# Performance work log

Measured on AMD Instinct MI355X. Metric: run time of the kernel, lower is better.

The kernel has to match this reference:

```python
import jax, jax.numpy as jnp
import numpy as np

C = 51  # num_relation


def setup_inputs() -> dict:
    key = jax.random.key(0)
    N_o, N_u, D = 16384, 16384, 1024
    k = jax.random.split(key, 6)
    feat = jax.random.normal(k[0], (N_o + N_u, D), jnp.float32)
    # first N_o rows are labeled (label != 0), remaining N_u rows unlabeled (label == 0)
    label = jnp.concatenate([
        jax.random.randint(k[1], (N_o,), 1, C),
        jnp.zeros((N_u,), jnp.int32),
    ]).astype(jnp.int32)
    W_o = jax.random.normal(k[2], (C, D), jnp.float32) * 0.03
    b_o = jnp.zeros((C,), jnp.float32)
    W = jax.random.normal(k[3], (C, D), jnp.float32) * 0.03
    b = jnp.zeros((C,), jnp.float32)
    cls = jnp.arange(C)
    group_mid_mask = (cls >= 16) & (cls < 36)   # groups[1]
    group_tail_mask = cls >= 36                 # groups[2]
    # runtime torch.randint partner sampling, hoisted to input construction
    idx_m = jax.random.randint(k[4], (2, N_u), 0, N_o)  # 2 mid copies
    idx_t = jax.random.randint(k[5], (3, N_u), 0, N_o)  # 3 tail copies
    return dict(feat=feat, label=label, W_o=W_o, b_o=b_o, W=W, b=b,
                group_mid_mask=group_mid_mask, group_tail_mask=group_tail_mask,
                idx_m=idx_m, idx_t=idx_t)


def reference(feat, label, W_o, b_o, W, b, group_mid_mask, group_tail_mask, idx_m, idx_t):
    n_u = idx_m.shape[1]
    n_o = feat.shape[0] - n_u
    feat_o, feat_u = feat[:n_o], feat[n_o:]
    label_o = label[:n_o]

    # fc_o under no_grad, then softmax / top-1 rank + score
    logits = jax.lax.stop_gradient(feat_u @ W_o.T + b_o)      # [N_u, C]
    p = jax.nn.softmax(logits, axis=1)
    pred = jnp.argmax(p, axis=1)                               # ranks[:,0]
    score = jnp.max(p, axis=1)                                 # score[:,0]

    # group membership + confidence thresholds (heads are unused in the original)
    mid_m = group_mid_mask[pred] & (score > 0.5)
    tail_m = group_tail_mask[pred] & (score > 0.3)

    oh_u = jax.nn.one_hot(pred, C, dtype=feat.dtype)
    oh_o = jax.nn.one_hot(label_o, C, dtype=feat.dtype)

    im = idx_m.reshape(-1)   # [2*N_u]
    it = idx_t.reshape(-1)   # [3*N_u]

    fm = 0.7 * feat_o[im] + 0.3 * jnp.tile(feat_u, (2, 1))
    lm = 0.7 * oh_o[im] + 0.3 * jnp.tile(oh_u, (2, 1))
    ft = 0.7 * feat_o[it] + 0.3 * jnp.tile(feat_u, (3, 1))
    lt = 0.7 * oh_o[it] + 0.3 * jnp.tile(oh_u, (3, 1))

    feat_cat = jnp.concatenate([fm, ft], axis=0)               # [5*N_u, D]
    label_cat = jnp.concatenate([lm, lt], axis=0)              # [5*N_u, C]
    w = jnp.concatenate([jnp.tile(mid_m, 2), jnp.tile(tail_m, 3)]).astype(feat.dtype)

    # soft-label cross entropy on fc(feat_cat); masked mean over selected rows
    logp = jax.nn.log_softmax(feat_cat @ W.T + b, axis=1)
    ce = -(logp * label_cat).sum(axis=1)
    cnt = w.sum()
    return (ce * w).sum() / jnp.maximum(cnt, 1.0)
```

## Files before the change

### kernel.cpp

```cpp
#include <hip/hip_runtime.h>
#include <math.h>

#define DD 1024
#define SN 52
#define NU 16384
#define NO 16384
#define CEBLK 5120

typedef short short8 __attribute__((ext_vector_type(8)));
typedef float f32x4 __attribute__((ext_vector_type(4)));

__device__ __forceinline__ unsigned short f2b(float x) {
    unsigned int u = __float_as_uint(x);
    u += 0x7FFFu + ((u >> 16) & 1u);
    return (unsigned short)(u >> 16);
}

__device__ __forceinline__ short8 cvt8(float4 a, float4 b) {
    short8 r;
    r[0] = (short)f2b(a.x); r[1] = (short)f2b(a.y);
    r[2] = (short)f2b(a.z); r[3] = (short)f2b(a.w);
    r[4] = (short)f2b(b.x); r[5] = (short)f2b(b.y);
    r[6] = (short)f2b(b.z); r[7] = (short)f2b(b.w);
    return r;
}

__device__ __forceinline__ void gl_lds(const void* g, void* l) {
    __builtin_amdgcn_global_load_lds(
        (const __attribute__((address_space(1))) void*)g,
        (__attribute__((address_space(3))) void*)l, 16, 0, 0);
}

__global__ __launch_bounds__(256) void convW(const float* __restrict__ W,
                                             const float* __restrict__ W_o,
                                             unsigned short* __restrict__ Wcat) {
    const int n = blockIdx.x;
    const int k = threadIdx.x * 4;
    const float* src = nullptr;
    if (n < 64) { if (n < 51) src = W + (size_t)n * DD; }
    else        { if (n - 64 < 51) src = W_o + (size_t)(n - 64) * DD; }
    float4 v = src ? *(const float4*)(src + k) : make_float4(0.f, 0.f, 0.f, 0.f);
    ushort4 o;
    o.x = f2b(v.x); o.y = f2b(v.y); o.z = f2b(v.z); o.w = f2b(v.w);
    *(ushort4*)(Wcat + (size_t)n * DD + k) = o;
}

template <int IS_U>
__device__ __forceinline__ void gemm_body(const float* __restrict__ feat,
                                          const unsigned short* __restrict__ Wcat,
                                          const float* __restrict__ b_o,
                                          int m0, float* __restrict__ Bmat,
                                          int* __restrict__ flags, char* lds) {
    const int tid = threadIdx.x;
    const int lane = tid & 63;
    const int w = tid >> 6;
    const int m = lane & 15;
    const int quad = lane >> 4;
    const int s = m & 7;
    const int s2 = m & 3;

    const char *gs0, *gs1, *gs2;
    int lo0, lo1, lo2, st1;
    if constexpr (!IS_U) {
        { const int r = w * 16 + (lane >> 3);
          const int g = (lane & 7) ^ (r & 7);
          gs0 = (const char*)(feat + (size_t)(m0 + r) * DD + g * 4); lo0 = (w * 2) * 1024; }
        { const int r = w * 16 + 8 + (lane >> 3);
          const int g = (lane & 7) ^ (r & 7);
          gs1 = (const char*)(feat + (size_t)(m0 + r) * DD + g * 4); lo1 = (w * 2 + 1) * 1024; }
        { const int r = w * 16 + (lane >> 2);
          const int g = (lane & 3) ^ (r & 3);
          gs2 = (const char*)(Wcat + (size_t)r * DD + g * 8); lo2 = 8192 + w * 1024; }
        st1 = 128;
    } else {
        { const int r = w * 8 + (lane >> 3);
          const int g = (lane & 7) ^ (r & 7);
          gs0 = (const char*)(feat + (size_t)(NO + m0 + r) * DD + g * 4); lo0 = w * 1024; }
        { const int r = (w * 2) * 16 + (lane >> 2);
          const int g = (lane & 3) ^ (r & 3);
          gs1 = (const char*)(Wcat + (size_t)r * DD + g * 8); lo1 = 4096 + (w * 2) * 1024; }
        { const int r = (w * 2 + 1) * 16 + (lane >> 2);
          const int g = (lane & 3) ^ (r & 3);
          gs2 = (const char*)(Wcat + (size_t)r * DD + g * 8); lo2 = 4096 + (w * 2 + 1) * 1024; }
        st1 = 64;
    }

    f32x4 acc[4];
#pragma unroll
    for (int nf = 0; nf < 4; ++nf) acc[nf] = (f32x4){0.f, 0.f, 0.f, 0.f};

    const int rA = (IS_U ? (w & 1) * 16 : w * 16) + m;
    const int rBbase = (IS_U ? (w >> 1) * 64 : 0) + m;
    const int Bofs = IS_U ? 4096 : 8192;

#define STAGE(t, buf)                                  \
    do {                                               \
        gl_lds(gs0 + (size_t)(t) * 128, (buf) + lo0);  \
        gl_lds(gs1 + (size_t)(t) * st1, (buf) + lo1);  \
        gl_lds(gs2 + (size_t)(t) * 64,  (buf) + lo2);  \
    } while (0)

    STAGE(0, lds);
    STAGE(1, lds + 12288);

    int bc = 0;
    for (int kt = 0; kt < 32; ++kt) {
        if (kt < 30) {
            const int bi2 = (bc == 0) ? 2 : bc - 1;
            STAGE(kt + 2, lds + bi2 * 12288);
            asm volatile("s_waitcnt vmcnt(6)\n\ts_barrier" ::: "memory");
        } else if (kt == 30) {
            asm volatile("s_waitcnt vmcnt(3)\n\ts_barrier" ::: "memory");
        } else {
            asm volatile("s_waitcnt vmcnt(0)\n\ts_barrier" ::: "memory");
        }
        const char* buf = lds + bc * 12288;
        const float4 f0 = *(const float4*)(buf + rA * 128 + ((2 * quad) ^ s) * 16);
        const float4 f1 = *(const float4*)(buf + rA * 128 + ((2 * quad + 1) ^ s) * 16);
        const short8 af = cvt8(f0, f1);
#pragma unroll
        for (int nf = 0; nf < 4; ++nf) {
            const short8 bf =
                *(const short8*)(buf + Bofs + (rBbase + nf * 16) * 64 + (quad ^ s2) * 16);
            acc[nf] = __builtin_amdgcn_mfma_f32_16x16x32_bf16(af, bf, acc[nf], 0, 0, 0);
        }
        bc = (bc == 2) ? 0 : bc + 1;
    }
#undef STAGE

    if constexpr (!IS_U) {
        const int rbase = m0 + w * 16 + quad * 4;
#pragma unroll
        for (int nf = 0; nf < 4; ++nf) {
            const int col = nf * 16 + m;
            if (col < 51) {
#pragma unroll
                for (int r = 0; r < 4; ++r)
                    Bmat[(size_t)(rbase + r) * SN + col] = acc[nf][r];
            }
        }
    } else {
        const int wm = w & 1, wn = w >> 1;
        const int rloc = m0 + wm * 16 + quad * 4;
        if (wn == 0) {
#pragma unroll
            for (int nf = 0; nf < 4; ++nf) {
                const int col = nf * 16 + m;
                if (col < 51) {
#pragma unroll
                    for (int r = 0; r < 4; ++r)
                        Bmat[(size_t)(NO + rloc + r) * SN + col] = acc[nf][r];
                }
            }
        } else {
            float boc[4];
#pragma unroll
            for (int c = 0; c < 4; ++c) {
                const int col = c * 16 + m;
                boc[c] = (col < 51) ? b_o[col] : 0.f;
            }
#pragma unroll
            for (int r = 0; r < 4; ++r) {
                float z[4];
                float mx = acc[0][r] + boc[0];
                int mi = m;
                z[0] = mx;
#pragma unroll
                for (int c = 1; c < 4; ++c) {
                    const int col = c * 16 + m;
                    z[c] = (col < 51) ? acc[c][r] + boc[c] : -INFINITY;
                    if (z[c] > mx) { mx = z[c]; mi = col; }
                }
#pragma unroll
                for (int off = 1; off < 16; off <<= 1) {
                    const float om = __shfl_xor(mx, off);
                    const int oi = __shfl_xor(mi, off);
                    if (om > mx || (om == mx && oi < mi)) { mx = om; mi = oi; }
                }
                float e = 0.f;
#pragma unroll
                for (int c = 0; c < 4; ++c)
                    if (c * 16 + m < 51) e += expf(z[c] - mx);
#pragma unroll
                for (int off = 1; off < 16; off <<= 1) e += __shfl_xor(e, off);
                const float score = 1.f / e;
                const int mid = (mi >= 16 && mi < 36 && score > 0.5f) ? 1 : 0;
                const int tail = (mi >= 36 && score > 0.3f) ? 1 : 0;
                if (m == 0) flags[rloc + r] = mi | (mid << 8) | (tail << 9);
            }
        }
    }
}

__global__ __launch_bounds__(256, 4) void gemm_mfma(const float* __restrict__ feat,
                                                    const unsigned short* __restrict__ Wcat,
                                                    const float* __restrict__ b_o,
                                                    float* __restrict__ Bmat,
                                                    int* __restrict__ flags) {
    __shared__ __attribute__((aligned(16))) char lds[3 * 12288];
    if (blockIdx.x < 256)
        gemm_body<0>(feat, Wcat, b_o, blockIdx.x * 64, Bmat, flags, lds);
    else
        gemm_body<1>(feat, Wcat, b_o, (blockIdx.x - 256) * 32, Bmat, flags, lds);
}

__global__ __launch_bounds__(256) void cekernel(const float* __restrict__ B,
                                                const float* __restrict__ bb,
                                                const int* __restrict__ label,
                                                const int* __restrict__ idxm,
                                                const int* __restrict__ idxt,
                                                const int* __restrict__ flags,
                                                double* __restrict__ pnum,
                                                int* __restrict__ pcnt) {
    __shared__ float snum[4];
    __shared__ int scnt[4];
    const int w = threadIdx.x >> 6;
    const int lane = threadIdx.x & 63;
    float csum = 0.f;
    int ccnt = 0;
#pragma unroll
    for (int it = 0; it < 4; ++it) {
        const int j = (blockIdx.x * 4 + w) * 4 + it;
        int u, o, active;
        if (j < 2 * NU) {
            u = j & (NU - 1);
            o = idxm[j];
            active = (flags[u] >> 8) & 1;
        } else {
            const int j2 = j - 2 * NU;
            u = j2 & (NU - 1);
            o = idxt[j2];
            active = (flags[u] >> 9) & 1;
        }
        if (active) {
            const float* Bo = B + (size_t)o * SN;
            const float* Bu = B + (size_t)(NO + u) * SN;
            float z = -INFINITY;
            if (lane < 51) z = 0.7f * Bo[lane] + 0.3f * Bu[lane] + bb[lane];
            float m = z;
#pragma unroll
            for (int off = 1; off < 64; off <<= 1) m = fmaxf(m, __shfl_xor(m, off));
            float e = (lane < 51) ? expf(z - m) : 0.f;
#pragma unroll
            for (int off = 1; off < 64; off <<= 1) e += __shfl_xor(e, off);
            const float lse = m + logf(e);
            const int lo = label[o];
            const int pu = flags[u] & 255;
            const float zlo = __shfl(z, lo);
            const float zpu = __shfl(z, pu);
            csum += lse - 0.7f * zlo - 0.3f * zpu;
            ccnt += 1;
        }
    }
    if (lane == 0) { snum[w] = csum; scnt[w] = ccnt; }
    __syncthreads();
    if (threadIdx.x == 0) {
        pnum[blockIdx.x] = (double)snum[0] + (double)snum[1] +
                           (double)snum[2] + (double)snum[3];
        pcnt[blockIdx.x] = scnt[0] + scnt[1] + scnt[2] + scnt[3];
    }
}

__global__ __launch_bounds__(256) void finalize(const double* __restrict__ pnum,
                                                const int* __restrict__ pcnt,
                                                float* __restrict__ out) {
    __shared__ double sd[4];
    __shared__ int sc[4];
    const int w = threadIdx.x >> 6;
    const int lane = threadIdx.x & 63;
    double s = 0.0;
    int c = 0;
    for (int i = threadIdx.x; i < CEBLK; i += 256) {
        s += pnum[i];
        c += pcnt[i];
    }
#pragma unroll
    for (int off = 1; off < 64; off <<= 1) {
        s += __shfl_xor(s, off);
        c += __shfl_xor(c, off);
    }
    if (lane == 0) { sd[w] = s; sc[w] = c; }
    __syncthreads();
    if (threadIdx.x == 0) {
        const double n = sd[0] + sd[1] + sd[2] + sd[3];
        const int cc = sc[0] + sc[1] + sc[2] + sc[3];
        out[0] = (float)(n / (cc > 1 ? (double)cc : 1.0));
    }
}

extern "C" void kernel_launch(void* const* d_in, const int* in_sizes, int n_in,
                              void* d_out, int out_size, void* d_ws, size_t ws_size,
                              hipStream_t stream) {
    const float* feat = (const float*)d_in[0];
    const int* label = (const int*)d_in[1];
    const float* W_o = (const float*)d_in[2];
    const float* b_o = (const float*)d_in[3];
    const float* W = (const float*)d_in[4];
    const float* b = (const float*)d_in[5];
    const int* idxm = (const int*)d_in[8];
    const int* idxt = (const int*)d_in[9];

    char* ws = (char*)d_ws;
    float* Bmat = (float*)ws;
    double* pnum = (double*)(ws + 6815744);
    int* pcnt = (int*)(ws + 6815744 + 40960);
    int* flags = (int*)(ws + 6815744 + 40960 + 20480);
    unsigned short* Wcat =
        (unsigned short*)(ws + 6815744 + 40960 + 20480 + 65536);

    convW<<<128, 256, 0, stream>>>(W, W_o, Wcat);
    gemm_mfma<<<768, 256, 0, stream>>>(feat, Wcat, b_o, Bmat, flags);
    cekernel<<<CEBLK, 256, 0, stream>>>(Bmat, b, label, idxm, idxt, flags, pnum, pcnt);
    finalize<<<1, 256, 0, stream>>>(pnum, pcnt, (float*)d_out);
}
```

Before: 237.2 us.

## Project only labeled rows referenced by active mixup pairs; ballot-compact CE work

Splits the fused GEMM into an unlabeled-row pass and a labeled-row pass. The unlabeled pass computes pseudo-labels and flags, then uses an atomic bitmap to build a deduplicated list of labeled rows that active mid/tail pairs actually reference. The labeled GEMM then gathers and projects only those rows instead of all 16384. The CE kernel now assigns one pair per lane and walks only the active lanes via a ballot mask, which cuts its block count. This adds atomics, an extra launch, and a gather with data-dependent work in exchange for skipping projections of unreferenced rows.

After: 243.7 us. +2.8%, slower.

```diff
diff --git a/kernel.cpp b/kernel.cpp
--- a/kernel.cpp
+++ b/kernel.cpp
@@ -5,7 +5,7 @@
 #define SN 52
 #define NU 16384
 #define NO 16384
-#define CEBLK 5120
+#define NCEB 320
 
 typedef short short8 __attribute__((ext_vector_type(8)));
 typedef float f32x4 __attribute__((ext_vector_type(4)));
@@ -33,7 +33,14 @@
 
 __global__ __launch_bounds__(256) void convW(const float* __restrict__ W,
                                              const float* __restrict__ W_o,
-                                             unsigned short* __restrict__ Wcat) {
+                                             unsigned short* __restrict__ Wcat,
+                                             unsigned int* __restrict__ bitmap,
+                                             int* __restrict__ cnt) {
+    if (blockIdx.x == 0) {
+        bitmap[threadIdx.x] = 0u;
+        bitmap[threadIdx.x + 256] = 0u;
+        if (threadIdx.x == 0) cnt[0] = 0;
+    }
     const int n = blockIdx.x;
     const int k = threadIdx.x * 4;
     const float* src = nullptr;
@@ -45,12 +52,18 @@
     *(ushort4*)(Wcat + (size_t)n * DD + k) = o;
 }
 
-template <int IS_U>
-__device__ __forceinline__ void gemm_body(const float* __restrict__ feat,
-                                          const unsigned short* __restrict__ Wcat,
-                                          const float* __restrict__ b_o,
-                                          int m0, float* __restrict__ Bmat,
-                                          int* __restrict__ flags, char* lds) {
+__global__ __launch_bounds__(256, 4) void gemm_u(const float* __restrict__ feat,
+                                                 const unsigned short* __restrict__ Wcat,
+                                                 const float* __restrict__ b_o,
+                                                 float* __restrict__ Bmat,
+                                                 int* __restrict__ flags,
+                                                 const int* __restrict__ idxm,
+                                                 const int* __restrict__ idxt,
+                                                 unsigned int* __restrict__ bitmap,
+                                                 int* __restrict__ cnt,
+                                                 int* __restrict__ listo) {
+    __shared__ __attribute__((aligned(16))) char lds[3 * 12288];
+    const int m0 = blockIdx.x * 32;
     const int tid = threadIdx.x;
     const int lane = tid & 63;
     const int w = tid >> 6;
@@ -60,54 +73,39 @@
     const int s2 = m & 3;
 
     const char *gs0, *gs1, *gs2;
-    int lo0, lo1, lo2, st1;
-    if constexpr (!IS_U) {
-        { const int r = w * 16 + (lane >> 3);
-          const int g = (lane & 7) ^ (r & 7);
-          gs0 = (const char*)(feat + (size_t)(m0 + r) * DD + g * 4); lo0 = (w * 2) * 1024; }
-        { const int r = w * 16 + 8 + (lane >> 3);
-          const int g = (lane & 7) ^ (r & 7);
-          gs1 = (const char*)(feat + (size_t)(m0 + r) * DD + g * 4); lo1 = (w * 2 + 1) * 1024; }
-        { const int r = w * 16 + (lane >> 2);
-          const int g = (lane & 3) ^ (r & 3);
-          gs2 = (const char*)(Wcat + (size_t)r * DD + g * 8); lo2 = 8192 + w * 1024; }
-        st1 = 128;
-    } else {
-        { const int r = w * 8 + (lane >> 3);
-          const int g = (lane & 7) ^ (r & 7);
-          gs0 = (const char*)(feat + (size_t)(NO + m0 + r) * DD + g * 4); lo0 = w * 1024; }
-        { const int r = (w * 2) * 16 + (lane >> 2);
-          const int g = (lane & 3) ^ (r & 3);
-          gs1 = (const char*)(Wcat + (size_t)r * DD + g * 8); lo1 = 4096 + (w * 2) * 1024; }
-        { const int r = (w * 2 + 1) * 16 + (lane >> 2);
-          const int g = (lane & 3) ^ (r & 3);
-          gs2 = (const char*)(Wcat + (size_t)r * DD + g * 8); lo2 = 4096 + (w * 2 + 1) * 1024; }
-        st1 = 64;
-    }
+    int lo0, lo1, lo2;
+    { const int r = w * 8 + (lane >> 3);
+      const int g = (lane & 7) ^ (r & 7);
+      gs0 = (const char*)(feat + (size_t)(NO + m0 + r) * DD + g * 4); lo0 = w * 1024; }
+    { const int r = (w * 2) * 16 + (lane >> 2);
+      const int g = (lane & 3) ^ (r & 3);
+      gs1 = (const char*)(Wcat + (size_t)r * DD + g * 8); lo1 = 4096 + (w * 2) * 1024; }
+    { const int r = (w * 2 + 1) * 16 + (lane >> 2);
+      const int g = (lane & 3) ^ (r & 3);
+      gs2 = (const char*)(Wcat + (size_t)r * DD + g * 8); lo2 = 4096 + (w * 2 + 1) * 1024; }
 
     f32x4 acc[4];
 #pragma unroll
     for (int nf = 0; nf < 4; ++nf) acc[nf] = (f32x4){0.f, 0.f, 0.f, 0.f};
 
-    const int rA = (IS_U ? (w & 1) * 16 : w * 16) + m;
-    const int rBbase = (IS_U ? (w >> 1) * 64 : 0) + m;
-    const int Bofs = IS_U ? 4096 : 8192;
-
-#define STAGE(t, buf)                                  \
+    const int rA = (w & 1) * 16 + m;
+    const int rBbase = (w >> 1) * 64 + m;
+
+#define STAGEU(t, buf)                                 \
     do {                                               \
         gl_lds(gs0 + (size_t)(t) * 128, (buf) + lo0);  \
-        gl_lds(gs1 + (size_t)(t) * st1, (buf) + lo1);  \
+        gl_lds(gs1 + (size_t)(t) * 64,  (buf) + lo1);  \
         gl_lds(gs2 + (size_t)(t) * 64,  (buf) + lo2);  \
     } while (0)
 
-    STAGE(0, lds);
-    STAGE(1, lds + 12288);
+    STAGEU(0, lds);
+    STAGEU(1, lds + 12288);
 
     int bc = 0;
     for (int kt = 0; kt < 32; ++kt) {
         if (kt < 30) {
             const int bi2 = (bc == 0) ? 2 : bc - 1;
-            STAGE(kt + 2, lds + bi2 * 12288);
+            STAGEU(kt + 2, lds + bi2 * 12288);
             asm volatile("s_waitcnt vmcnt(6)\n\ts_barrier" ::: "memory");
         } else if (kt == 30) {
             asm volatile("s_waitcnt vmcnt(3)\n\ts_barrier" ::: "memory");
@@ -121,87 +119,167 @@
 #pragma unroll
         for (int nf = 0; nf < 4; ++nf) {
             const short8 bf =
-                *(const short8*)(buf + Bofs + (rBbase + nf * 16) * 64 + (quad ^ s2) * 16);
+                *(const short8*)(buf + 4096 + (rBbase + nf * 16) * 64 + (quad ^ s2) * 16);
             acc[nf] = __builtin_amdgcn_mfma_f32_16x16x32_bf16(af, bf, acc[nf], 0, 0, 0);
         }
         bc = (bc == 2) ? 0 : bc + 1;
     }
-#undef STAGE
-
-    if constexpr (!IS_U) {
-        const int rbase = m0 + w * 16 + quad * 4;
+#undef STAGEU
+
+    const int wm = w & 1, wn = w >> 1;
+    const int rloc = m0 + wm * 16 + quad * 4;
+    if (wn == 0) {
 #pragma unroll
         for (int nf = 0; nf < 4; ++nf) {
             const int col = nf * 16 + m;
             if (col < 51) {
 #pragma unroll
                 for (int r = 0; r < 4; ++r)
-                    Bmat[(size_t)(rbase + r) * SN + col] = acc[nf][r];
+                    Bmat[(size_t)(NO + rloc + r) * SN + col] = acc[nf][r];
             }
         }
     } else {
-        const int wm = w & 1, wn = w >> 1;
-        const int rloc = m0 + wm * 16 + quad * 4;
-        if (wn == 0) {
-#pragma unroll
-            for (int nf = 0; nf < 4; ++nf) {
-                const int col = nf * 16 + m;
-                if (col < 51) {
-#pragma unroll
-                    for (int r = 0; r < 4; ++r)
-                        Bmat[(size_t)(NO + rloc + r) * SN + col] = acc[nf][r];
+        float boc[4];
+#pragma unroll
+        for (int c = 0; c < 4; ++c) {
+            const int col = c * 16 + m;
+            boc[c] = (col < 51) ? b_o[col] : 0.f;
+        }
+#pragma unroll
+        for (int r = 0; r < 4; ++r) {
+            float z[4];
+            float mx = acc[0][r] + boc[0];
+            int mi = m;
+            z[0] = mx;
+#pragma unroll
+            for (int c = 1; c < 4; ++c) {
+                const int col = c * 16 + m;
+                z[c] = (col < 51) ? acc[c][r] + boc[c] : -INFINITY;
+                if (z[c] > mx) { mx = z[c]; mi = col; }
+            }
+#pragma unroll
+            for (int off = 1; off < 16; off <<= 1) {
+                const float om = __shfl_xor(mx, off);
+                const int oi = __shfl_xor(mi, off);
+                if (om > mx || (om == mx && oi < mi)) { mx = om; mi = oi; }
+            }
+            float e = 0.f;
+#pragma unroll
+            for (int c = 0; c < 4; ++c)
+                if (c * 16 + m < 51) e += expf(z[c] - mx);
+#pragma unroll
+            for (int off = 1; off < 16; off <<= 1) e += __shfl_xor(e, off);
+            const float score = 1.f / e;
+            const int mid = (mi >= 16 && mi < 36 && score > 0.5f) ? 1 : 0;
+            const int tail = (mi >= 36 && score > 0.3f) ? 1 : 0;
+            if (m == 0) flags[rloc + r] = mi | (mid << 8) | (tail << 9);
+            const int nref = mid ? 2 : (tail ? 3 : 0);
+            if (m < nref) {
+                const int u = rloc + r;
+                const int oo = mid ? idxm[(size_t)m * NU + u]
+                                   : idxt[(size_t)m * NU + u];
+                const unsigned bit = 1u << (oo & 31);
+                const unsigned old = atomicOr(&bitmap[oo >> 5], bit);
+                if (!(old & bit)) {
+                    const int p = atomicAdd(cnt, 1);
+                    listo[p] = oo;
                 }
             }
+        }
+    }
+}
+
+__global__ __launch_bounds__(256, 4) void gemm_o(const float* __restrict__ feat,
+                                                 const unsigned short* __restrict__ Wcat,
+                                                 float* __restrict__ Bmat,
+                                                 const int* __restrict__ cnt,
+                                                 const int* __restrict__ listo) {
+    const int n = cnt[0];
+    const int base = blockIdx.x * 64;
+    if (base >= n) return;
+    __shared__ __attribute__((aligned(16))) char lds[3 * 12288];
+    const int nm1 = n - 1;
+    const int tid = threadIdx.x;
+    const int lane = tid & 63;
+    const int w = tid >> 6;
+    const int m = lane & 15;
+    const int quad = lane >> 4;
+    const int s = m & 7;
+    const int s2 = m & 3;
+
+    const char *gs0, *gs1, *gs2;
+    int lo0, lo1, lo2;
+    { const int r = w * 16 + (lane >> 3);
+      const int g = (lane & 7) ^ (r & 7);
+      int li = base + r; if (li > nm1) li = nm1;
+      const int gr = listo[li];
+      gs0 = (const char*)(feat + (size_t)gr * DD + g * 4); lo0 = (w * 2) * 1024; }
+    { const int r = w * 16 + 8 + (lane >> 3);
+      const int g = (lane & 7) ^ (r & 7);
+      int li = base + r; if (li > nm1) li = nm1;
+      const int gr = listo[li];
+      gs1 = (const char*)(feat + (size_t)gr * DD + g * 4); lo1 = (w * 2 + 1) * 1024; }
+    { const int r = w * 16 + (lane >> 2);
+      const int g = (lane & 3) ^ (r & 3);
+      gs2 = (const char*)(Wcat + (size_t)r * DD + g * 8); lo2 = 8192 + w * 1024; }
+
+    f32x4 acc[4];
+#pragma unroll
+    for (int nf = 0; nf < 4; ++nf) acc[nf] = (f32x4){0.f, 0.f, 0.f, 0.f};
+
+    const int rA = w * 16 + m;
+
+#define STAGEO(t, buf)                                 \
+    do {                                               \
+        gl_lds(gs0 + (size_t)(t) * 128, (buf) + lo0);  \
+        gl_lds(gs1 + (size_t)(t) * 128, (buf) + lo1);  \
+        gl_lds(gs2 + (size_t)(t) * 64,  (buf) + lo2);  \
+    } while (0)
+
+    STAGEO(0, lds);
+    STAGEO(1, lds + 12288);
+
+    int bc = 0;
+    for (int kt = 0; kt < 32; ++kt) {
+        if (kt < 30) {
+            const int bi2 = (bc == 0) ? 2 : bc - 1;
+            STAGEO(kt + 2, lds + bi2 * 12288);
+            asm volatile("s_waitcnt vmcnt(6)\n\ts_barrier" ::: "memory");
+        } else if (kt == 30) {
+            asm volatile("s_waitcnt vmcnt(3)\n\ts_barrier" ::: "memory");
         } else {
-            float boc[4];
-#pragma unroll
-            for (int c = 0; c < 4; ++c) {
-                const int col = c * 16 + m;
-                boc[c] = (col < 51) ? b_o[col] : 0.f;
-            }
-#pragma unroll
-            for (int r = 0; r < 4; ++r) {
-                float z[4];
-                float mx = acc[0][r] + boc[0];
-                int mi = m;
-                z[0] = mx;
-#pragma unroll
-                for (int c = 1; c < 4; ++c) {
-                    const int col = c * 16 + m;
-                    z[c] = (col < 51) ? acc[c][r] + boc[c] : -INFINITY;
-                    if (z[c] > mx) { mx = z[c]; mi = col; }
-                }
-#pragma unroll
-                for (int off = 1; off < 16; off <<= 1) {
-                    const float om = __shfl_xor(mx, off);
-                    const int oi = __shfl_xor(mi, off);
-                    if (om > mx || (om == mx && oi < mi)) { mx = om; mi = oi; }
-                }
-                float e = 0.f;
-#pragma unroll
-                for (int c = 0; c < 4; ++c)
-                    if (c * 16 + m < 51) e += expf(z[c] - mx);
-#pragma unroll
-                for (int off = 1; off < 16; off <<= 1) e += __shfl_xor(e, off);
-                const float score = 1.f / e;
-                const int mid = (mi >= 16 && mi < 36 && score > 0.5f) ? 1 : 0;
-                const int tail = (mi >= 36 && score > 0.3f) ? 1 : 0;
-                if (m == 0) flags[rloc + r] = mi | (mid << 8) | (tail << 9);
-            }
-        }
-    }
-}
-
-__global__ __launch_bounds__(256, 4) void gemm_mfma(const float* __restrict__ feat,
-                                                    const unsigned short* __restrict__ Wcat,
-                                                    const float* __restrict__ b_o,
-                                                    float* __restrict__ Bmat,
-                                                    int* __restrict__ flags) {
-    __shared__ __attribute__((aligned(16))) char lds[3 * 12288];
-    if (blockIdx.x < 256)
-        gemm_body<0>(feat, Wcat, b_o, blockIdx.x * 64, Bmat, flags, lds);
-    else
-        gemm_body<1>(feat, Wcat, b_o, (blockIdx.x - 256) * 32, Bmat, flags, lds);
+            asm volatile("s_waitcnt vmcnt(0)\n\ts_barrier" ::: "memory");
+        }
+        const char* buf = lds + bc * 12288;
+        const float4 f0 = *(const float4*)(buf + rA * 128 + ((2 * quad) ^ s) * 16);
+        const float4 f1 = *(const float4*)(buf + rA * 128 + ((2 * quad + 1) ^ s) * 16);
+        const short8 af = cvt8(f0, f1);
+#pragma unroll
+        for (int nf = 0; nf < 4; ++nf) {
+            const short8 bf =
+                *(const short8*)(buf + 8192 + (m + nf * 16) * 64 + (quad ^ s2) * 16);
+            acc[nf] = __builtin_amdgcn_mfma_f32_16x16x32_bf16(af, bf, acc[nf], 0, 0, 0);
+        }
+        bc = (bc == 2) ? 0 : bc + 1;
+    }
+#undef STAGEO
+
+    const int rl = w * 16 + quad * 4;
+    int grow[4];
+#pragma unroll
+    for (int r = 0; r < 4; ++r) {
+        int li = base + rl + r; if (li > nm1) li = nm1;
+        grow[r] = listo[li];
+    }
+#pragma unroll
+    for (int nf = 0; nf < 4; ++nf) {
+        const int col = nf * 16 + m;
+        if (col < 51) {
+#pragma unroll
+            for (int r = 0; r < 4; ++r)
+                Bmat[(size_t)grow[r] * SN + col] = acc[nf][r];
+        }
+    }
 }
 
 __global__ __launch_bounds__(256) void cekernel(const float* __restrict__ B,
@@ -216,43 +294,48 @@
     __shared__ int scnt[4];
     const int w = threadIdx.x >> 6;
     const int lane = threadIdx.x & 63;
-    float csum = 0.f;
+    const int j = (blockIdx.x * 4 + w) * 64 + lane;
+    int u, o, fl, act;
+    if (j < 2 * NU) {
+        u = j & (NU - 1);
+        fl = flags[u];
+        act = (fl >> 8) & 1;
+        o = idxm[j];
+    } else {
+        const int j2 = j - 2 * NU;
+        u = j2 & (NU - 1);
+        fl = flags[u];
+        act = (fl >> 9) & 1;
+        o = idxt[j2];
+    }
+    const float bbv = (lane < 51) ? bb[lane] : 0.f;
+    unsigned long long mask = __ballot(act);
+    float fsum = 0.f;
     int ccnt = 0;
-#pragma unroll
-    for (int it = 0; it < 4; ++it) {
-        const int j = (blockIdx.x * 4 + w) * 4 + it;
-        int u, o, active;
-        if (j < 2 * NU) {
-            u = j & (NU - 1);
-            o = idxm[j];
-            active = (flags[u] >> 8) & 1;
-        } else {
-            const int j2 = j - 2 * NU;
-            u = j2 & (NU - 1);
-            o = idxt[j2];
-            active = (flags[u] >> 9) & 1;
-        }
-        if (active) {
-            const float* Bo = B + (size_t)o * SN;
-            const float* Bu = B + (size_t)(NO + u) * SN;
-            float z = -INFINITY;
-            if (lane < 51) z = 0.7f * Bo[lane] + 0.3f * Bu[lane] + bb[lane];
-            float m = z;
-#pragma unroll
-            for (int off = 1; off < 64; off <<= 1) m = fmaxf(m, __shfl_xor(m, off));
-            float e = (lane < 51) ? expf(z - m) : 0.f;
-#pragma unroll
-            for (int off = 1; off < 64; off <<= 1) e += __shfl_xor(e, off);
-            const float lse = m + logf(e);
-            const int lo = label[o];
-            const int pu = flags[u] & 255;
-            const float zlo = __shfl(z, lo);
-            const float zpu = __shfl(z, pu);
-            csum += lse - 0.7f * zlo - 0.3f * zpu;
-            ccnt += 1;
-        }
-    }
-    if (lane == 0) { snum[w] = csum; scnt[w] = ccnt; }
+    while (mask) {
+        const int b = (int)__builtin_ctzll(mask);
+        mask &= mask - 1;
+        const int ob = __shfl(o, b);
+        const int ub = __shfl(u, b);
+        const int pu = __shfl(fl, b) & 255;
+        float z = -INFINITY;
+        if (lane < 51)
+            z = 0.7f * B[(size_t)ob * SN + lane] +
+                0.3f * B[(size_t)(NO + ub) * SN + lane] + bbv;
+        float mx = z;
+#pragma unroll
+        for (int off = 1; off < 64; off <<= 1) mx = fmaxf(mx, __shfl_xor(mx, off));
+        float e = (lane < 51) ? expf(z - mx) : 0.f;
+#pragma unroll
+        for (int off = 1; off < 64; off <<= 1) e += __shfl_xor(e, off);
+        const float lse = mx + logf(e);
+        const int lo = label[ob];
+        const float zlo = __shfl(z, lo);
+        const float zpu = __shfl(z, pu);
+        fsum += lse - 0.7f * zlo - 0.3f * zpu;
+        ++ccnt;
+    }
+    if (lane == 0) { snum[w] = fsum; scnt[w] = ccnt; }
     __syncthreads();
     if (threadIdx.x == 0) {
         pnum[blockIdx.x] = (double)snum[0] + (double)snum[1] +
@@ -270,7 +353,7 @@
     const int lane = threadIdx.x & 63;
     double s = 0.0;
     int c = 0;
-    for (int i = threadIdx.x; i < CEBLK; i += 256) {
+    for (int i = threadIdx.x; i < NCEB; i += 256) {
         s += pnum[i];
         c += pcnt[i];
     }
@@ -303,13 +386,17 @@
     char* ws = (char*)d_ws;
     float* Bmat = (float*)ws;
     double* pnum = (double*)(ws + 6815744);
-    int* pcnt = (int*)(ws + 6815744 + 40960);
-    int* flags = (int*)(ws + 6815744 + 40960 + 20480);
-    unsigned short* Wcat =
-        (unsigned short*)(ws + 6815744 + 40960 + 20480 + 65536);
-
-    convW<<<128, 256, 0, stream>>>(W, W_o, Wcat);
-    gemm_mfma<<<768, 256, 0, stream>>>(feat, Wcat, b_o, Bmat, flags);
-    cekernel<<<CEBLK, 256, 0, stream>>>(Bmat, b, label, idxm, idxt, flags, pnum, pcnt);
+    int* pcnt = (int*)(ws + 6818304);
+    int* flags = (int*)(ws + 6819584);
+    unsigned short* Wcat = (unsigned short*)(ws + 6885120);
+    unsigned int* bitmap = (unsigned int*)(ws + 7147264);
+    int* cntp = (int*)(ws + 7149312);
+    int* listo = (int*)(ws + 7149328);
+
+    convW<<<128, 256, 0, stream>>>(W, W_o, Wcat, bitmap, cntp);
+    gemm_u<<<512, 256, 0, stream>>>(feat, Wcat, b_o, Bmat, flags, idxm, idxt,
+                                    bitmap, cntp, listo);
+    gemm_o<<<256, 256, 0, stream>>>(feat, Wcat, Bmat, cntp, listo);
+    cekernel<<<NCEB, 256, 0, stream>>>(Bmat, b, label, idxm, idxt, flags, pnum, pcnt);
     finalize<<<1, 256, 0, stream>>>(pnum, pcnt, (float*)d_out);
 }
```

## Compute CE logits only for active mixup rows and drop the labeled GEMM

Applied to the files above, without the earlier changes.

The full bf16 GEMM over the labeled rows, the stored logit matrix and the separate finalize kernel are removed. The GEMM now runs only over the unlabeled rows to produce pseudo-label flags. The CE kernel ballots which mixup rows pass the confidence mask. For each such row it builds the mixed feature and computes its 51 logits with fp32 dot products against W inside the wave. A global atomic accumulator with a last-block-done counter replaces the finalize pass. Cost now depends on how many rows are active, and per-row wave-serial dot products could be slow if many rows pass the threshold.

Result: no change. 239.1 us (+0.8%).

```diff
diff --git a/kernel.cpp b/kernel.cpp
--- a/kernel.cpp
+++ b/kernel.cpp
@@ -2,10 +2,9 @@
 #include <math.h>
 
 #define DD 1024
-#define SN 52
 #define NU 16384
 #define NO 16384
-#define CEBLK 5120
+#define NCEB 320
 
 typedef short short8 __attribute__((ext_vector_type(8)));
 typedef float f32x4 __attribute__((ext_vector_type(4)));
@@ -31,26 +30,29 @@
         (__attribute__((address_space(3))) void*)l, 16, 0, 0);
 }
 
-__global__ __launch_bounds__(256) void convW(const float* __restrict__ W,
-                                             const float* __restrict__ W_o,
-                                             unsigned short* __restrict__ Wcat) {
+__global__ __launch_bounds__(256) void convW(const float* __restrict__ W_o,
+                                             unsigned short* __restrict__ Wcat,
+                                             double* __restrict__ gnum,
+                                             int* __restrict__ gcnt,
+                                             int* __restrict__ gdone) {
+    if (blockIdx.x == 0 && threadIdx.x == 0) {
+        gnum[0] = 0.0; gcnt[0] = 0; gdone[0] = 0;
+    }
     const int n = blockIdx.x;
     const int k = threadIdx.x * 4;
-    const float* src = nullptr;
-    if (n < 64) { if (n < 51) src = W + (size_t)n * DD; }
-    else        { if (n - 64 < 51) src = W_o + (size_t)(n - 64) * DD; }
+    const float* src = (n < 51) ? (W_o + (size_t)n * DD) : nullptr;
     float4 v = src ? *(const float4*)(src + k) : make_float4(0.f, 0.f, 0.f, 0.f);
     ushort4 o;
     o.x = f2b(v.x); o.y = f2b(v.y); o.z = f2b(v.z); o.w = f2b(v.w);
     *(ushort4*)(Wcat + (size_t)n * DD + k) = o;
 }
 
-template <int IS_U>
-__device__ __forceinline__ void gemm_body(const float* __restrict__ feat,
-                                          const unsigned short* __restrict__ Wcat,
-                                          const float* __restrict__ b_o,
-                                          int m0, float* __restrict__ Bmat,
-                                          int* __restrict__ flags, char* lds) {
+__global__ __launch_bounds__(256, 4) void gemm_u(const float* __restrict__ feat,
+                                                 const unsigned short* __restrict__ Wcat,
+                                                 const float* __restrict__ b_o,
+                                                 int* __restrict__ flags) {
+    __shared__ __attribute__((aligned(16))) char lds[3 * 12288];
+    const int m0 = blockIdx.x * 64;
     const int tid = threadIdx.x;
     const int lane = tid & 63;
     const int w = tid >> 6;
@@ -60,43 +62,27 @@
     const int s2 = m & 3;
 
     const char *gs0, *gs1, *gs2;
-    int lo0, lo1, lo2, st1;
-    if constexpr (!IS_U) {
-        { const int r = w * 16 + (lane >> 3);
-          const int g = (lane & 7) ^ (r & 7);
-          gs0 = (const char*)(feat + (size_t)(m0 + r) * DD + g * 4); lo0 = (w * 2) * 1024; }
-        { const int r = w * 16 + 8 + (lane >> 3);
-          const int g = (lane & 7) ^ (r & 7);
-          gs1 = (const char*)(feat + (size_t)(m0 + r) * DD + g * 4); lo1 = (w * 2 + 1) * 1024; }
-        { const int r = w * 16 + (lane >> 2);
-          const int g = (lane & 3) ^ (r & 3);
-          gs2 = (const char*)(Wcat + (size_t)r * DD + g * 8); lo2 = 8192 + w * 1024; }
-        st1 = 128;
-    } else {
-        { const int r = w * 8 + (lane >> 3);
-          const int g = (lane & 7) ^ (r & 7);
-          gs0 = (const char*)(feat + (size_t)(NO + m0 + r) * DD + g * 4); lo0 = w * 1024; }
-        { const int r = (w * 2) * 16 + (lane >> 2);
-          const int g = (lane & 3) ^ (r & 3);
-          gs1 = (const char*)(Wcat + (size_t)r * DD + g * 8); lo1 = 4096 + (w * 2) * 1024; }
-        { const int r = (w * 2 + 1) * 16 + (lane >> 2);
-          const int g = (lane & 3) ^ (r & 3);
-          gs2 = (const char*)(Wcat + (size_t)r * DD + g * 8); lo2 = 4096 + (w * 2 + 1) * 1024; }
-        st1 = 64;
-    }
+    int lo0, lo1, lo2;
+    { const int r = w * 16 + (lane >> 3);
+      const int g = (lane & 7) ^ (r & 7);
+      gs0 = (const char*)(feat + (size_t)(NO + m0 + r) * DD + g * 4); lo0 = (w * 2) * 1024; }
+    { const int r = w * 16 + 8 + (lane >> 3);
+      const int g = (lane & 7) ^ (r & 7);
+      gs1 = (const char*)(feat + (size_t)(NO + m0 + r) * DD + g * 4); lo1 = (w * 2 + 1) * 1024; }
+    { const int r = w * 16 + (lane >> 2);
+      const int g = (lane & 3) ^ (r & 3);
+      gs2 = (const char*)(Wcat + (size_t)r * DD + g * 8); lo2 = 8192 + w * 1024; }
 
     f32x4 acc[4];
 #pragma unroll
     for (int nf = 0; nf < 4; ++nf) acc[nf] = (f32x4){0.f, 0.f, 0.f, 0.f};
 
-    const int rA = (IS_U ? (w & 1) * 16 : w * 16) + m;
-    const int rBbase = (IS_U ? (w >> 1) * 64 : 0) + m;
-    const int Bofs = IS_U ? 4096 : 8192;
+    const int rA = w * 16 + m;
 
 #define STAGE(t, buf)                                  \
     do {                                               \
         gl_lds(gs0 + (size_t)(t) * 128, (buf) + lo0);  \
-        gl_lds(gs1 + (size_t)(t) * st1, (buf) + lo1);  \
+        gl_lds(gs1 + (size_t)(t) * 128, (buf) + lo1);  \
         gl_lds(gs2 + (size_t)(t) * 64,  (buf) + lo2);  \
     } while (0)
 
@@ -121,170 +107,138 @@
 #pragma unroll
         for (int nf = 0; nf < 4; ++nf) {
             const short8 bf =
-                *(const short8*)(buf + Bofs + (rBbase + nf * 16) * 64 + (quad ^ s2) * 16);
+                *(const short8*)(buf + 8192 + (m + nf * 16) * 64 + (quad ^ s2) * 16);
             acc[nf] = __builtin_amdgcn_mfma_f32_16x16x32_bf16(af, bf, acc[nf], 0, 0, 0);
         }
         bc = (bc == 2) ? 0 : bc + 1;
     }
 #undef STAGE
 
-    if constexpr (!IS_U) {
-        const int rbase = m0 + w * 16 + quad * 4;
-#pragma unroll
-        for (int nf = 0; nf < 4; ++nf) {
-            const int col = nf * 16 + m;
-            if (col < 51) {
-#pragma unroll
-                for (int r = 0; r < 4; ++r)
-                    Bmat[(size_t)(rbase + r) * SN + col] = acc[nf][r];
-            }
-        }
-    } else {
-        const int wm = w & 1, wn = w >> 1;
-        const int rloc = m0 + wm * 16 + quad * 4;
-        if (wn == 0) {
-#pragma unroll
-            for (int nf = 0; nf < 4; ++nf) {
-                const int col = nf * 16 + m;
-                if (col < 51) {
-#pragma unroll
-                    for (int r = 0; r < 4; ++r)
-                        Bmat[(size_t)(NO + rloc + r) * SN + col] = acc[nf][r];
-                }
-            }
-        } else {
-            float boc[4];
-#pragma unroll
-            for (int c = 0; c < 4; ++c) {
-                const int col = c * 16 + m;
-                boc[c] = (col < 51) ? b_o[col] : 0.f;
-            }
-#pragma unroll
-            for (int r = 0; r < 4; ++r) {
-                float z[4];
-                float mx = acc[0][r] + boc[0];
-                int mi = m;
-                z[0] = mx;
-#pragma unroll
-                for (int c = 1; c < 4; ++c) {
-                    const int col = c * 16 + m;
-                    z[c] = (col < 51) ? acc[c][r] + boc[c] : -INFINITY;
-                    if (z[c] > mx) { mx = z[c]; mi = col; }
-                }
-#pragma unroll
-                for (int off = 1; off < 16; off <<= 1) {
-                    const float om = __shfl_xor(mx, off);
-                    const int oi = __shfl_xor(mi, off);
-                    if (om > mx || (om == mx && oi < mi)) { mx = om; mi = oi; }
-                }
-                float e = 0.f;
-#pragma unroll
-                for (int c = 0; c < 4; ++c)
-                    if (c * 16 + m < 51) e += expf(z[c] - mx);
-#pragma unroll
-                for (int off = 1; off < 16; off <<= 1) e += __shfl_xor(e, off);
-                const float score = 1.f / e;
-                const int mid = (mi >= 16 && mi < 36 && score > 0.5f) ? 1 : 0;
-                const int tail = (mi >= 36 && score > 0.3f) ? 1 : 0;
-                if (m == 0) flags[rloc + r] = mi | (mid << 8) | (tail << 9);
-            }
-        }
-    }
-}
-
-__global__ __launch_bounds__(256, 4) void gemm_mfma(const float* __restrict__ feat,
-                                                    const unsigned short* __restrict__ Wcat,
-                                                    const float* __restrict__ b_o,
-                                                    float* __restrict__ Bmat,
-                                                    int* __restrict__ flags) {
-    __shared__ __attribute__((aligned(16))) char lds[3 * 12288];
-    if (blockIdx.x < 256)
-        gemm_body<0>(feat, Wcat, b_o, blockIdx.x * 64, Bmat, flags, lds);
-    else
-        gemm_body<1>(feat, Wcat, b_o, (blockIdx.x - 256) * 32, Bmat, flags, lds);
-}
-
-__global__ __launch_bounds__(256) void cekernel(const float* __restrict__ B,
+    const int rloc = m0 + w * 16 + quad * 4;
+    float boc[4];
+#pragma unroll
+    for (int c = 0; c < 4; ++c) {
+        const int col = c * 16 + m;
+        boc[c] = (col < 51) ? b_o[col] : 0.f;
+    }
+#pragma unroll
+    for (int r = 0; r < 4; ++r) {
+        float z[4];
+        float mx = acc[0][r] + boc[0];
+        int mi = m;
+        z[0] = mx;
+#pragma unroll
+        for (int c = 1; c < 4; ++c) {
+            const int col = c * 16 + m;
+            z[c] = (col < 51) ? acc[c][r] + boc[c] : -INFINITY;
+            if (z[c] > mx) { mx = z[c]; mi = col; }
+        }
+#pragma unroll
+        for (int off = 1; off < 16; off <<= 1) {
+            const float om = __shfl_xor(mx, off);
+            const int oi = __shfl_xor(mi, off);
+            if (om > mx || (om == mx && oi < mi)) { mx = om; mi = oi; }
+        }
+        float e = 0.f;
+#pragma unroll
+        for (int c = 0; c < 4; ++c)
+            if (c * 16 + m < 51) e += expf(z[c] - mx);
+#pragma unroll
+        for (int off = 1; off < 16; off <<= 1) e += __shfl_xor(e, off);
+        const float score = 1.f / e;
+        const int mid = (mi >= 16 && mi < 36 && score > 0.5f) ? 1 : 0;
+        const int tail = (mi >= 36 && score > 0.3f) ? 1 : 0;
+        if (m == 0) flags[rloc + r] = mi | (mid << 8) | (tail << 9);
+    }
+}
+
+__global__ __launch_bounds__(256) void cekernel(const float* __restrict__ feat,
+                                                const float* __restrict__ W,
                                                 const float* __restrict__ bb,
                                                 const int* __restrict__ label,
                                                 const int* __restrict__ idxm,
                                                 const int* __restrict__ idxt,
                                                 const int* __restrict__ flags,
-                                                double* __restrict__ pnum,
-                                                int* __restrict__ pcnt) {
+                                                double* __restrict__ gnum,
+                                                int* __restrict__ gcnt,
+                                                int* __restrict__ gdone,
+                                                float* __restrict__ out) {
     __shared__ float snum[4];
     __shared__ int scnt[4];
     const int w = threadIdx.x >> 6;
     const int lane = threadIdx.x & 63;
-    float csum = 0.f;
+    const int j = (blockIdx.x * 4 + w) * 64 + lane;
+    int u, o, fl, act;
+    if (j < 2 * NU) {
+        u = j & (NU - 1);
+        fl = flags[u];
+        act = (fl >> 8) & 1;
+        o = idxm[j];
+    } else {
+        const int j2 = j - 2 * NU;
+        u = j2 & (NU - 1);
+        fl = flags[u];
+        act = (fl >> 9) & 1;
+        o = idxt[j2];
+    }
+    const float bbv = (lane < 51) ? bb[lane] : 0.f;
+    unsigned long long mask = __ballot(act);
+    float fsum = 0.f;
     int ccnt = 0;
-#pragma unroll
-    for (int it = 0; it < 4; ++it) {
-        const int j = (blockIdx.x * 4 + w) * 4 + it;
-        int u, o, active;
-        if (j < 2 * NU) {
-            u = j & (NU - 1);
-            o = idxm[j];
-            active = (flags[u] >> 8) & 1;
-        } else {
-            const int j2 = j - 2 * NU;
-            u = j2 & (NU - 1);
-            o = idxt[j2];
-            active = (flags[u] >> 9) & 1;
-        }
-        if (active) {
-            const float* Bo = B + (size_t)o * SN;
-            const float* Bu = B + (size_t)(NO + u) * SN;
-            float z = -INFINITY;
-            if (lane < 51) z = 0.7f * Bo[lane] + 0.3f * Bu[lane] + bb[lane];
-            float m = z;
-#pragma unroll
-            for (int off = 1; off < 64; off <<= 1) m = fmaxf(m, __shfl_xor(m, off));
-            float e = (lane < 51) ? expf(z - m) : 0.f;
-#pragma unroll
-            for (int off = 1; off < 64; off <<= 1) e += __shfl_xor(e, off);
-            const float lse = m + logf(e);
-            const int lo = label[o];
-            const int pu = flags[u] & 255;
-            const float zlo = __shfl(z, lo);
-            const float zpu = __shfl(z, pu);
-            csum += lse - 0.7f * zlo - 0.3f * zpu;
-            ccnt += 1;
-        }
-    }
-    if (lane == 0) { snum[w] = csum; scnt[w] = ccnt; }
+    while (mask) {
+        const int bpos = (int)__builtin_ctzll(mask);
+        mask &= mask - 1;
+        const int ob = __shfl(o, bpos);
+        const int ub = __shfl(u, bpos);
+        const int pu = __shfl(fl, bpos) & 255;
+        const f32x4* fo4 = (const f32x4*)(feat + (size_t)ob * DD);
+        const f32x4* fu4 = (const f32x4*)(feat + (size_t)(NO + ub) * DD);
+        f32x4 g[4];
+#pragma unroll
+        for (int t = 0; t < 4; ++t)
+            g[t] = 0.7f * fo4[t * 64 + lane] + 0.3f * fu4[t * 64 + lane];
+        float zmy = 0.f;
+        for (int c = 0; c < 51; ++c) {
+            const f32x4* wr = (const f32x4*)(W + (size_t)c * DD);
+            f32x4 p = wr[lane] * g[0];
+            p += wr[64 + lane] * g[1];
+            p += wr[128 + lane] * g[2];
+            p += wr[192 + lane] * g[3];
+            float d = (p[0] + p[1]) + (p[2] + p[3]);
+#pragma unroll
+            for (int off = 1; off < 64; off <<= 1) d += __shfl_xor(d, off);
+            if (lane == c) zmy = d;
+        }
+        const float z = (lane < 51) ? zmy + bbv : -INFINITY;
+        float mx = z;
+#pragma unroll
+        for (int off = 1; off < 64; off <<= 1) mx = fmaxf(mx, __shfl_xor(mx, off));
+        float e = (lane < 51) ? expf(z - mx) : 0.f;
+#pragma unroll
+        for (int off = 1; off < 64; off <<= 1) e += __shfl_xor(e, off);
+        const float lse = mx + logf(e);
+        const int lo = label[ob];
+        const float zlo = __shfl(z, lo);
+        const float zpu = __shfl(z, pu);
+        fsum += lse - 0.7f * zlo - 0.3f * zpu;
+        ++ccnt;
+    }
+    if (lane == 0) { snum[w] = fsum; scnt[w] = ccnt; }
     __syncthreads();
     if (threadIdx.x == 0) {
-        pnum[blockIdx.x] = (double)snum[0] + (double)snum[1] +
-                           (double)snum[2] + (double)snum[3];
-        pcnt[blockIdx.x] = scnt[0] + scnt[1] + scnt[2] + scnt[3];
-    }
-}
-
-__global__ __launch_bounds__(256) void finalize(const double* __restrict__ pnum,
-                                                const int* __restrict__ pcnt,
-                                                float* __restrict__ out) {
-    __shared__ double sd[4];
-    __shared__ int sc[4];
-    const int w = threadIdx.x >> 6;
-    const int lane = threadIdx.x & 63;
-    double s = 0.0;
-    int c = 0;
-    for (int i = threadIdx.x; i < CEBLK; i += 256) {
-        s += pnum[i];
-        c += pcnt[i];
-    }
-#pragma unroll
-    for (int off = 1; off < 64; off <<= 1) {
-        s += __shfl_xor(s, off);
-        c += __shfl_xor(c, off);
-    }
-    if (lane == 0) { sd[w] = s; sc[w] = c; }
-    __syncthreads();
-    if (threadIdx.x == 0) {
-        const double n = sd[0] + sd[1] + sd[2] + sd[3];
-        const int cc = sc[0] + sc[1] + sc[2] + sc[3];
-        out[0] = (float)(n / (cc > 1 ? (double)cc : 1.0));
+        const float bn = snum[0] + snum[1] + snum[2] + snum[3];
+        const int bcnt = scnt[0] + scnt[1] + scnt[2] + scnt[3];
+        if (bcnt > 0) {
+            atomicAdd(gnum, (double)bn);
+            atomicAdd(gcnt, bcnt);
+        }
+        __threadfence();
+        const int dn = atomicAdd(gdone, 1);
+        if (dn == NCEB - 1) {
+            const double n = atomicAdd(gnum, 0.0);
+            const int cc = atomicAdd(gcnt, 0);
+            out[0] = (float)(n / (cc > 1 ? (double)cc : 1.0));
+        }
     }
 }
 
@@ -301,15 +255,14 @@
     const int* idxt = (const int*)d_in[9];
 
     char* ws = (char*)d_ws;
-    float* Bmat = (float*)ws;
-    double* pnum = (double*)(ws + 6815744);
-    int* pcnt = (int*)(ws + 6815744 + 40960);
-    int* flags = (int*)(ws + 6815744 + 40960 + 20480);
-    unsigned short* Wcat =
-        (unsigned short*)(ws + 6815744 + 40960 + 20480 + 65536);
-
-    convW<<<128, 256, 0, stream>>>(W, W_o, Wcat);
-    gemm_mfma<<<768, 256, 0, stream>>>(feat, Wcat, b_o, Bmat, flags);
-    cekernel<<<CEBLK, 256, 0, stream>>>(Bmat, b, label, idxm, idxt, flags, pnum, pcnt);
-    finalize<<<1, 256, 0, stream>>>(pnum, pcnt, (float*)d_out);
-}
+    int* flags = (int*)ws;
+    unsigned short* Wcat = (unsigned short*)(ws + 65536);
+    double* gnum = (double*)(ws + 196608);
+    int* gcnt = (int*)(ws + 196616);
+    int* gdone = (int*)(ws + 196620);
+
+    convW<<<64, 256, 0, stream>>>(W_o, Wcat, gnum, gcnt, gdone);
+    gemm_u<<<256, 256, 0, stream>>>(feat, Wcat, b_o, flags);
+    cekernel<<<NCEB, 256, 0, stream>>>(feat, W, b, label, idxm, idxt, flags,
+                                       gnum, gcnt, gdone, (float*)d_out);
+}
```
